# Optimization experiments

Measured on AMD Instinct MI355X. Metric: run time of the kernel, lower is better.

The kernel has to match this reference:

```python
import jax, jax.numpy as jnp
import numpy as np

GRID_MIN, GRID_MAX = -3.0, 3.0
N_AXIS = 64            # 64x64 grid -> m = 4096
LENGTHSCALE = 0.5      # RBF kernel lengthscale
EPS = 1e-6


def make_grid():
    lin = jnp.linspace(GRID_MIN, GRID_MAX, N_AXIS, dtype=jnp.float32)
    gx, gy = jnp.meshgrid(lin, lin, indexing='ij')
    return jnp.stack([gx.ravel(), gy.ravel()], axis=-1)  # [m, 2]


def setup_inputs() -> dict:
    key = jax.random.key(0)
    k1, k2 = jax.random.split(key)
    X = jax.random.normal(k1, (16, 1024, 2), dtype=jnp.float32)  # context locations
    Y = jax.random.normal(k2, (16, 1024, 8), dtype=jnp.float32)  # context values
    return {"X": X, "Y": Y}


def reference(X, Y):
    grid = make_grid()                                   # [m, 2]
    # expand_with_ones: prepend a ones channel (density channel)
    ones = jnp.ones(Y.shape[:-1] + (1,), dtype=Y.dtype)
    Yb = jnp.concatenate([ones, Y], axis=-1)             # [b, n, 1+dy]

    # kernel_smooth: RBF kernel between grid and X, contracted with Yb.
    # squared distances via the expanded form (avoids [b,m,n,2] intermediate)
    g2 = jnp.sum(grid * grid, axis=-1)                   # [m]
    x2 = jnp.sum(X * X, axis=-1)                         # [b, n]
    gx = jnp.einsum('md,bnd->bmn', grid, X)              # [b, m, n]
    d2 = g2[None, :, None] + x2[:, None, :] - 2.0 * gx   # [b, m, n]
    K = jnp.exp(-d2 / (2.0 * LENGTHSCALE * LENGTHSCALE)) # [b, m, n]

    Y_grid = jnp.einsum('bmn,bnc->bmc', K, Yb)           # [b, m, 1+dy]

    # normalise: divide feature channels by the density channel
    density = Y_grid[:, :, :1]
    feats = Y_grid[:, :, 1:] / (density + EPS)
    Y_grid = jnp.concatenate([density, feats], axis=-1)

    return grid[None], Y_grid
```

## Files before the change

kernel.cpp:

```cpp
#include <hip/hip_runtime.h>

typedef _Float16 half8   __attribute__((ext_vector_type(8)));
typedef float    floatx4 __attribute__((ext_vector_type(4)));

#define STEP  (6.0f / 63.0f)
#define SCAL  1.69864636f

__global__ __launch_bounds__(512, 2) void rkhs_fused(
    const float* __restrict__ X,
    const float* __restrict__ Y,
    float* __restrict__ out)
{
    __shared__ __align__(16) unsigned char smem[65536];
    float*    sXy   = (float*)smem;
    _Float16* sEx   = (_Float16*)(smem + 4096);
    floatx4*  spark = (floatx4*)smem;
    float*    sfin  = (float*)smem;

    const int b   = blockIdx.x >> 4;
    const int rw  = blockIdx.x & 15;
    const int tid = threadIdx.x;
    const int w   = tid >> 6, l = tid & 63, q = l >> 4, n = l & 15;
    const int r0  = rw * 4;

    {
        const float2 v0 = ((const float2*)X)[b * 1024 + 2 * tid];
        const float2 v1 = ((const float2*)X)[b * 1024 + 2 * tid + 1];
        sXy[2 * tid]     = SCAL * v0.y;
        sXy[2 * tid + 1] = SCAL * v1.y;
    }

    if (b == 0) {
        const int row = r0 + (tid >> 7), rem = tid & 127;
        out[(size_t)rw * 512 + tid] = (rem & 1)
            ? (-3.0f + (float)(rem >> 1) * STEP)
            : (-3.0f + (float)row * STEP);
    }

    half8 ybr[4];
#pragma unroll
    for (int ss = 0; ss < 4; ++ss) {
        half8 h;
        if (n == 0) {
#pragma unroll
            for (int j = 0; j < 8; ++j) h[j] = (_Float16)1.0f;
        } else if (n <= 8) {
            const float* yp = Y + ((size_t)(b * 1024 + (w * 4 + ss) * 32 + q * 8)) * 8 + (n - 1);
#pragma unroll
            for (int j = 0; j < 8; ++j) h[j] = (_Float16)yp[j * 8];
        } else {
#pragma unroll
            for (int j = 0; j < 8; ++j) h[j] = (_Float16)0.0f;
        }
        ybr[ss] = h;
    }

    if (tid < 128) {
        const int s = tid >> 2, rr = tid & 3;
        const float gS = SCAL * (-3.0f + (float)(r0 + rr) * STEP);
        const float* xp = X + (size_t)(b * 1024 + s * 32) * 2;
#pragma unroll
        for (int g = 0; g < 4; ++g) {
            half8 hbuf;
#pragma unroll
            for (int j = 0; j < 8; ++j) {
                const float d = fmaf(-SCAL, xp[(g * 8 + j) * 2], gS);
                hbuf[j] = (_Float16)__builtin_amdgcn_exp2f(-(d * d));
            }
            *(half8*)(sEx + (s * 4 + rr) * 32 + g * 8) = hbuf;
        }
    }
    __syncthreads();

    float gSct[4];
#pragma unroll
    for (int ct = 0; ct < 4; ++ct)
        gSct[ct] = SCAL * (-3.0f + (float)(ct * 16 + n) * STEP);

    floatx4 acc[4][4];
#pragma unroll
    for (int rr = 0; rr < 4; ++rr)
#pragma unroll
        for (int ct = 0; ct < 4; ++ct) acc[rr][ct] = (floatx4){0.f, 0.f, 0.f, 0.f};

#pragma unroll
    for (int ss = 0; ss < 4; ++ss) {
        const int s   = w * 4 + ss;
        const int k0q = s * 32 + q * 8;
        const float4 xa = *(const float4*)(sXy + k0q);
        const float4 xb = *(const float4*)(sXy + k0q + 4);
        const float xk[8] = {xa.x, xa.y, xa.z, xa.w, xb.x, xb.y, xb.z, xb.w};

        half8 bp[4];
#pragma unroll
        for (int rr = 0; rr < 4; ++rr)
            bp[rr] = (*(const half8*)(sEx + (s * 4 + rr) * 32 + q * 8)) * ybr[ss];

#pragma unroll
        for (int ct = 0; ct < 4; ++ct) {
            half8 ey;
#pragma unroll
            for (int j = 0; j < 8; ++j) {
                const float d = gSct[ct] - xk[j];
                ey[j] = (_Float16)__builtin_amdgcn_exp2f(-(d * d));
            }
#pragma unroll
            for (int rr = 0; rr < 4; ++rr)
                acc[rr][ct] = __builtin_amdgcn_mfma_f32_16x16x32_f16(ey, bp[rr], acc[rr][ct], 0, 0, 0);
        }
    }
    __syncthreads();

#define PARKA(slot)                                                        \
    { _Pragma("unroll") for (int rr = 0; rr < 4; ++rr)                     \
      _Pragma("unroll") for (int ct = 0; ct < 4; ++ct)                     \
          spark[(slot) * 1024 + (rr * 4 + ct) * 64 + l] = acc[rr][ct]; }
#define ABSORBA(slot)                                                      \
    { _Pragma("unroll") for (int rr = 0; rr < 4; ++rr)                     \
      _Pragma("unroll") for (int ct = 0; ct < 4; ++ct)                     \
          acc[rr][ct] += spark[(slot) * 1024 + (rr * 4 + ct) * 64 + l]; }

    if (w >= 4) PARKA(w - 4)
    __syncthreads();
    if (w < 4)  ABSORBA(w)
    __syncthreads();
    if (w == 2 || w == 3) PARKA(w - 2)
    __syncthreads();
    if (w < 2)  ABSORBA(w)
    __syncthreads();
    if (w == 1) PARKA(0)
    __syncthreads();

    if (w == 0) {
        ABSORBA(0)
#pragma unroll
        for (int rr = 0; rr < 4; ++rr)
#pragma unroll
            for (int ct = 0; ct < 4; ++ct)
                if (n < 9)
#pragma unroll
                    for (int i = 0; i < 4; ++i)
                        sfin[(rr * 64 + ct * 16 + q * 4 + i) * 9 + n] = acc[rr][ct][i];
    }
#undef PARKA
#undef ABSORBA
    __syncthreads();

    const size_t obase = 8192 + ((size_t)b * 4096 + (size_t)r0 * 64) * 9;
#pragma unroll
    for (int it = 0; it < 5; ++it) {
        const int idx = it * 512 + tid;
        if (idx < 2304) {
            const int m  = idx / 9;
            const int ch = idx - m * 9;
            const float dens = sfin[m * 9];
            const float v    = sfin[idx];
            out[obase + idx] = ch ? v * __builtin_amdgcn_rcpf(dens + 1e-6f) : dens;
        }
    }
}

extern "C" void kernel_launch(void* const* d_in, const int* in_sizes, int n_in,
                              void* d_out, int out_size, void* d_ws, size_t ws_size,
                              hipStream_t stream) {
    const float* X = (const float*)d_in[0];
    const float* Y = (const float*)d_in[1];
    float* out = (float*)d_out;
    (void)d_ws; (void)ws_size;

    rkhs_fused<<<dim3(256), dim3(512), 0, stream>>>(X, Y, out);
}
```

Measured before the change: 62.70 us.

## Spread row-exponential precompute over all threads and pack fp16 conversions

```diff
diff --git a/kernel.cpp b/kernel.cpp
--- a/kernel.cpp
+++ b/kernel.cpp
@@ -1,7 +1,12 @@
 #include <hip/hip_runtime.h>
 
-typedef _Float16 half8   __attribute__((ext_vector_type(8)));
+typedef _Float16 half8 __attribute__((ext_vector_type(8)));
+typedef __fp16   h2 __attribute__((ext_vector_type(2)));
+typedef __fp16   h4 __attribute__((ext_vector_type(4)));
+typedef __fp16   h8 __attribute__((ext_vector_type(8)));
 typedef float    floatx4 __attribute__((ext_vector_type(4)));
+typedef float    fv2 __attribute__((ext_vector_type(2)));
+typedef float    fv4 __attribute__((ext_vector_type(4)));
 
 #define STEP  (6.0f / 63.0f)
 #define SCAL  1.69864636f
@@ -12,8 +17,9 @@
     float* __restrict__ out)
 {
     __shared__ __align__(16) unsigned char smem[65536];
-    float*    sXy   = (float*)smem;
-    _Float16* sEx   = (_Float16*)(smem + 4096);
+    float*    sXx   = (float*)smem;
+    float*    sXy   = (float*)(smem + 4096);
+    _Float16* sEx   = (_Float16*)(smem + 8192);
     floatx4*  spark = (floatx4*)smem;
     float*    sfin  = (float*)smem;
 
@@ -23,11 +29,17 @@
     const int w   = tid >> 6, l = tid & 63, q = l >> 4, n = l & 15;
     const int r0  = rw * 4;
 
-    {
-        const float2 v0 = ((const float2*)X)[b * 1024 + 2 * tid];
-        const float2 v1 = ((const float2*)X)[b * 1024 + 2 * tid + 1];
-        sXy[2 * tid]     = SCAL * v0.y;
-        sXy[2 * tid + 1] = SCAL * v1.y;
+    const fv4 xv = *(const fv4*)(X + (size_t)b * 2048 + tid * 4);
+
+    float ybf[4][8];
+    const bool ldy = (n >= 1 && n <= 8);
+    if (ldy) {
+#pragma unroll
+        for (int ss = 0; ss < 4; ++ss) {
+            const float* yp = Y + ((size_t)(b * 1024 + (w * 4 + ss) * 32 + q * 8)) * 8 + (n - 1);
+#pragma unroll
+            for (int j = 0; j < 8; ++j) ybf[ss][j] = yp[j * 8];
+        }
     }
 
     if (b == 0) {
@@ -37,6 +49,32 @@
             : (-3.0f + (float)row * STEP);
     }
 
+    sXx[2 * tid]     = SCAL * xv[0];
+    sXy[2 * tid]     = SCAL * xv[1];
+    sXx[2 * tid + 1] = SCAL * xv[2];
+    sXy[2 * tid + 1] = SCAL * xv[3];
+    __syncthreads();
+
+    {
+        const int s = tid >> 4, rr = (tid >> 2) & 3, g = tid & 3;
+        const float gS = SCAL * (-3.0f + (float)(r0 + rr) * STEP);
+        const float* xp = sXx + s * 32 + g * 8;
+        h2 p[4];
+#pragma unroll
+        for (int hh = 0; hh < 4; ++hh) {
+            const float d0 = gS - xp[2 * hh];
+            const float d1 = gS - xp[2 * hh + 1];
+            p[hh] = __builtin_amdgcn_cvt_pkrtz(
+                __builtin_amdgcn_exp2f(-(d0 * d0)),
+                __builtin_amdgcn_exp2f(-(d1 * d1)));
+        }
+        const h8 packed = __builtin_shufflevector(
+            __builtin_shufflevector(p[0], p[1], 0, 1, 2, 3),
+            __builtin_shufflevector(p[2], p[3], 0, 1, 2, 3),
+            0, 1, 2, 3, 4, 5, 6, 7);
+        *(half8*)(sEx + (s * 4 + rr) * 32 + g * 8) = __builtin_bit_cast(half8, packed);
+    }
+
     half8 ybr[4];
 #pragma unroll
     for (int ss = 0; ss < 4; ++ss) {
@@ -44,31 +82,14 @@
         if (n == 0) {
 #pragma unroll
             for (int j = 0; j < 8; ++j) h[j] = (_Float16)1.0f;
-        } else if (n <= 8) {
-            const float* yp = Y + ((size_t)(b * 1024 + (w * 4 + ss) * 32 + q * 8)) * 8 + (n - 1);
-#pragma unroll
-            for (int j = 0; j < 8; ++j) h[j] = (_Float16)yp[j * 8];
+        } else if (ldy) {
+#pragma unroll
+            for (int j = 0; j < 8; ++j) h[j] = (_Float16)ybf[ss][j];
         } else {
 #pragma unroll
             for (int j = 0; j < 8; ++j) h[j] = (_Float16)0.0f;
         }
         ybr[ss] = h;
-    }
-
-    if (tid < 128) {
-        const int s = tid >> 2, rr = tid & 3;
-        const float gS = SCAL * (-3.0f + (float)(r0 + rr) * STEP);
-        const float* xp = X + (size_t)(b * 1024 + s * 32) * 2;
-#pragma unroll
-        for (int g = 0; g < 4; ++g) {
-            half8 hbuf;
-#pragma unroll
-            for (int j = 0; j < 8; ++j) {
-                const float d = fmaf(-SCAL, xp[(g * 8 + j) * 2], gS);
-                hbuf[j] = (_Float16)__builtin_amdgcn_exp2f(-(d * d));
-            }
-            *(half8*)(sEx + (s * 4 + rr) * 32 + g * 8) = hbuf;
-        }
     }
     __syncthreads();
 
@@ -87,9 +108,13 @@
     for (int ss = 0; ss < 4; ++ss) {
         const int s   = w * 4 + ss;
         const int k0q = s * 32 + q * 8;
-        const float4 xa = *(const float4*)(sXy + k0q);
-        const float4 xb = *(const float4*)(sXy + k0q + 4);
-        const float xk[8] = {xa.x, xa.y, xa.z, xa.w, xb.x, xb.y, xb.z, xb.w};
+        const fv4 xa = *(const fv4*)(sXy + k0q);
+        const fv4 xb = *(const fv4*)(sXy + k0q + 4);
+        fv2 xk2[4];
+        xk2[0] = __builtin_shufflevector(xa, xa, 0, 1);
+        xk2[1] = __builtin_shufflevector(xa, xa, 2, 3);
+        xk2[2] = __builtin_shufflevector(xb, xb, 0, 1);
+        xk2[3] = __builtin_shufflevector(xb, xb, 2, 3);
 
         half8 bp[4];
 #pragma unroll
@@ -98,12 +123,21 @@
 
 #pragma unroll
         for (int ct = 0; ct < 4; ++ct) {
-            half8 ey;
-#pragma unroll
-            for (int j = 0; j < 8; ++j) {
-                const float d = gSct[ct] - xk[j];
-                ey[j] = (_Float16)__builtin_amdgcn_exp2f(-(d * d));
+            const fv2 gS2 = {gSct[ct], gSct[ct]};
+            h2 p[4];
+#pragma unroll
+            for (int hh = 0; hh < 4; ++hh) {
+                const fv2 d  = gS2 - xk2[hh];
+                const fv2 dd = d * d;
+                p[hh] = __builtin_amdgcn_cvt_pkrtz(
+                    __builtin_amdgcn_exp2f(-dd[0]),
+                    __builtin_amdgcn_exp2f(-dd[1]));
             }
+            const h8 packed = __builtin_shufflevector(
+                __builtin_shufflevector(p[0], p[1], 0, 1, 2, 3),
+                __builtin_shufflevector(p[2], p[3], 0, 1, 2, 3),
+                0, 1, 2, 3, 4, 5, 6, 7);
+            const half8 ey = __builtin_bit_cast(half8, packed);
 #pragma unroll
             for (int rr = 0; rr < 4; ++rr)
                 acc[rr][ct] = __builtin_amdgcn_mfma_f32_16x16x32_f16(ey, bp[rr], acc[rr][ct], 0, 0, 0);
```

Result: no change. 62.18 us (-0.8%).
